# Kernel optimization log

Measured on AMD Instinct MI355X. Metric: run time of the kernel, lower is better.

The kernel has to match this reference:

```python
import jax, jax.numpy as jnp
import numpy as np

B, S = 1024, 64          # batch, num clips (att_size)
R = 1024                 # CG_rnn_size
E = 1024                 # CG_input_encoding_size
CD = 1024                # clip_context_dim
ED = 1024                # event_context_dim
H = 512                  # CG_att_hid_size


def setup_inputs() -> dict:
    key = jax.random.key(0)
    ks = jax.random.split(key, 20)
    s = 0.02
    return {
        "xt": jax.random.normal(ks[0], (B, E), jnp.float32),
        "video": jax.random.normal(ks[1], (B, 1024), jnp.float32),
        "event": jax.random.normal(ks[2], (B, ED), jnp.float32),
        "clip": jax.random.normal(ks[3], (B, S, CD), jnp.float32),
        "clip_mask": jax.random.randint(ks[4], (B, S), 0, 2, jnp.int32),
        "state_h": jax.random.normal(ks[5], (2, B, R), jnp.float32),
        "state_c": jax.random.normal(ks[6], (2, B, R), jnp.float32),
        # LSTMCell 0 (input = event ++ xt -> ED+E)
        "W_ih0": jax.random.normal(ks[7], (4 * R, ED + E), jnp.float32) * s,
        "b_ih0": jnp.zeros((4 * R,), jnp.float32),
        "W_hh0": jax.random.normal(ks[8], (4 * R, R), jnp.float32) * s,
        "b_hh0": jnp.zeros((4 * R,), jnp.float32),
        # LSTMCell 1 (input = att ++ xt -> CD+E)
        "W_ih1": jax.random.normal(ks[9], (4 * R, CD + E), jnp.float32) * s,
        "b_ih1": jnp.zeros((4 * R,), jnp.float32),
        "W_hh1": jax.random.normal(ks[10], (4 * R, R), jnp.float32) * s,
        "b_hh1": jnp.zeros((4 * R,), jnp.float32),
        # Attention params
        "W_ctx": jax.random.normal(ks[11], (H, CD), jnp.float32) * s,
        "b_ctx": jnp.zeros((H,), jnp.float32),
        "W_h2a": jax.random.normal(ks[12], (H, R), jnp.float32) * s,
        "b_h2a": jnp.zeros((H,), jnp.float32),
        "W_alpha": jax.random.normal(ks[13], (1, H), jnp.float32) * s,
        "b_alpha": jnp.zeros((1,), jnp.float32),
    }


def _lstm_cell(x, h, c, W_ih, b_ih, W_hh, b_hh):
    gates = x @ W_ih.T + b_ih + h @ W_hh.T + b_hh  # [B, 4R]
    i, f, g, o = jnp.split(gates, 4, axis=-1)
    i, f, o = jax.nn.sigmoid(i), jax.nn.sigmoid(f), jax.nn.sigmoid(o)
    g = jnp.tanh(g)
    c_new = f * c + i * g
    h_new = o * jnp.tanh(c_new)
    return h_new, c_new


def _attention(h, att_feats, att_mask, W_ctx, b_ctx, W_h2a, b_h2a, W_alpha, b_alpha):
    att = att_feats @ W_ctx.T + b_ctx                 # [B, S, H]
    att_h = h @ W_h2a.T + b_h2a                       # [B, H]
    dot = jnp.tanh(att + att_h[:, None, :])           # [B, S, H]
    scores = (dot @ W_alpha.T + b_alpha)[..., 0]      # [B, S]
    weight = jax.nn.softmax(scores, axis=1)
    m = att_mask.astype(weight.dtype)
    weight = weight * m
    weight = weight / jnp.sum(weight, axis=1, keepdims=True)
    return jnp.einsum('bs,bsd->bd', weight, att_feats)  # [B, CD]


def reference(xt, video, event, clip, clip_mask, state_h, state_c,
              W_ih0, b_ih0, W_hh0, b_hh0, W_ih1, b_ih1, W_hh1, b_hh1,
              W_ctx, b_ctx, W_h2a, b_h2a, W_alpha, b_alpha):
    pre_h1 = state_h[1]
    # stream 0: torch.cat((xt, event), 1)
    h0, c0 = _lstm_cell(jnp.concatenate([xt, event], axis=1),
                        state_h[0], state_c[0], W_ih0, b_ih0, W_hh0, b_hh0)
    att = _attention(pre_h1, clip, clip_mask,
                     W_ctx, b_ctx, W_h2a, b_h2a, W_alpha, b_alpha)
    h1, c1 = _lstm_cell(jnp.concatenate([xt, att], axis=1),
                        state_h[1], state_c[1], W_ih1, b_ih1, W_hh1, b_hh1)
    # dropout layers are identity in eval mode
    output = jnp.concatenate([h0, h1], axis=1)        # [B, 2R]
    new_h = jnp.stack([h0, h1])
    new_c = jnp.stack([c0, c1])
    return output, new_h, new_c
```

## Files before the change

kernel.cpp:

```cpp
#include <hip/hip_runtime.h>

typedef short short8 __attribute__((ext_vector_type(8)));
typedef float floatx4 __attribute__((ext_vector_type(4)));
typedef unsigned short u16;

__device__ __forceinline__ u16 cvt_bf(float x) {
  unsigned u = __float_as_uint(x);
  unsigned r = 0x7FFFu + ((u >> 16) & 1u);
  return (u16)((u + r) >> 16);
}
__device__ __forceinline__ float bf2f(u16 h) {
  return __uint_as_float(((unsigned)h) << 16);
}
__device__ __forceinline__ void gll16(const u16* g, u16* l) {
  __builtin_amdgcn_global_load_lds(
      (__attribute__((address_space(1))) void*)(void*)const_cast<u16*>(g),
      (__attribute__((address_space(3))) void*)(void*)l, 16, 0, 0);
}
__device__ __forceinline__ float fast_tanh(float x) {
  float t = __expf(-2.f * fabsf(x));
  float r = 1.f - 2.f * t / (1.f + t);
  return copysignf(r, x);
}
__device__ __forceinline__ float fast_sigm(float x) {
  return 1.f / (1.f + __expf(-x));
}

#define MAXSEG 13
struct ConvArgs {
  const float* src[MAXSEG];
  u16* dst[MAXSEG];
  unsigned lw[MAXSEG];
  unsigned dstride[MAXSEG];
  unsigned blk0[MAXSEG + 1];
  int nseg;
};
__global__ __launch_bounds__(256)
void convert_seg(ConvArgs a) {
  const unsigned blk = blockIdx.x;
  int s = 0;
  for (int i = 1; i < a.nseg; ++i) if (blk >= a.blk0[i]) s = i;
  const unsigned e0 = (blk - a.blk0[s]) * 2048u + threadIdx.x * 8u;
  short8 p = {};
  u16* d;
  const float* src = a.src[s];
  if (src) {
    const float4 v0 = *(const float4*)(src + e0);
    const float4 v1 = *(const float4*)(src + e0 + 4);
    const unsigned row = e0 >> a.lw[s];
    const unsigned col = e0 & ((1u << a.lw[s]) - 1u);
    d = a.dst[s] + (size_t)row * a.dstride[s] + col;
    p[0] = (short)cvt_bf(v0.x); p[1] = (short)cvt_bf(v0.y);
    p[2] = (short)cvt_bf(v0.z); p[3] = (short)cvt_bf(v0.w);
    p[4] = (short)cvt_bf(v1.x); p[5] = (short)cvt_bf(v1.y);
    p[6] = (short)cvt_bf(v1.z); p[7] = (short)cvt_bf(v1.w);
  } else {
    d = a.dst[s] + e0;
  }
  *(short8*)d = p;
}
__global__ __launch_bounds__(256)
void conv_flat(const float* __restrict__ src, u16* __restrict__ dst) {
  const size_t e = (size_t)blockIdx.x * 2048 + threadIdx.x * 8;
  const float4 v0 = *(const float4*)(src + e);
  const float4 v1 = *(const float4*)(src + e + 4);
  short8 p;
  p[0] = (short)cvt_bf(v0.x); p[1] = (short)cvt_bf(v0.y);
  p[2] = (short)cvt_bf(v0.z); p[3] = (short)cvt_bf(v0.w);
  p[4] = (short)cvt_bf(v1.x); p[5] = (short)cvt_bf(v1.y);
  p[6] = (short)cvt_bf(v1.z); p[7] = (short)cvt_bf(v1.w);
  *(short8*)(dst + e) = p;
}
__global__ __launch_bounds__(256)
void zerof(float* __restrict__ p) { p[blockIdx.x * 256 + threadIdx.x] = 0.f; }

__device__ __forceinline__ void gemm_body(
    const u16* __restrict__ A, int sa, const u16* __restrict__ B, int sb,
    int K, int Mbase, int Nbase, u16* sA, u16* sB, floatx4 (&acc)[4][4])
{
  const int tid = threadIdx.x, lane = tid & 63, w = tid >> 6;
  const int quad = lane >> 4, l15 = lane & 15;
  const int wm = w >> 1, wn = w & 1;
  const int srow = lane >> 3;
  const int sslot = (lane & 7) ^ srow;

  for (int k0 = 0; k0 < K; k0 += 64) {
    __syncthreads();
#pragma unroll
    for (int j = 0; j < 4; ++j) {
      const int c = w + 4 * j;
      const int row = c * 8 + srow;
      gll16(A + (size_t)(Mbase + row) * sa + k0 + sslot * 8, &sA[c * 512]);
      gll16(B + (size_t)(Nbase + row) * sb + k0 + sslot * 8, &sB[c * 512]);
    }
    __syncthreads();
#pragma unroll
    for (int ks = 0; ks < 2; ++ks) {
      short8 af[4], bf[4];
#pragma unroll
      for (int mt = 0; mt < 4; ++mt) {
        const int row = wm * 64 + mt * 16 + l15;
        af[mt] = *(const short8*)&sA[row * 64 + ((ks * 4 + quad) ^ (row & 7)) * 8];
      }
#pragma unroll
      for (int nt = 0; nt < 4; ++nt) {
        const int row = wn * 64 + nt * 16 + l15;
        bf[nt] = *(const short8*)&sB[row * 64 + ((ks * 4 + quad) ^ (row & 7)) * 8];
      }
#pragma unroll
      for (int mt = 0; mt < 4; ++mt)
#pragma unroll
        for (int nt = 0; nt < 4; ++nt)
          acc[mt][nt] = __builtin_amdgcn_mfma_f32_16x16x32_bf16(af[mt], bf[nt], acc[mt][nt], 0, 0, 0);
    }
  }
}

__device__ __forceinline__ void epi_store(
    floatx4 (&acc)[4][4], const float* __restrict__ bias0,
    const float* __restrict__ bias1, float* __restrict__ out,
    int N, int Mbase, int Nbase)
{
  const int tid = threadIdx.x, lane = tid & 63, w = tid >> 6;
  const int quad = lane >> 4, l15 = lane & 15;
  const int wm = w >> 1, wn = w & 1;
#pragma unroll
  for (int nt = 0; nt < 4; ++nt) {
    const int col = Nbase + wn * 64 + nt * 16 + l15;
    const float bc = bias0 ? (bias0[col] + bias1[col]) : 0.f;
#pragma unroll
    for (int mt = 0; mt < 4; ++mt) {
      const int rb = Mbase + wm * 64 + mt * 16 + quad * 4;
#pragma unroll
      for (int r = 0; r < 4; ++r)
        out[(size_t)(rb + r) * N + col] = acc[mt][nt][r] + bc;
    }
  }
}

__device__ __forceinline__ void epi_score(
    floatx4 (&acc)[4][4], const float* __restrict__ atth,
    const float* __restrict__ Walpha, float* __restrict__ scores,
    int Mbase, int Nbase)
{
  const int tid = threadIdx.x, lane = tid & 63, w = tid >> 6;
  const int quad = lane >> 4, l15 = lane & 15;
  const int wm = w >> 1, wn = w & 1;
  const int b = (Mbase + wm * 64) >> 6;
  float rs[4][4] = {};
#pragma unroll
  for (int nt = 0; nt < 4; ++nt) {
    const int col = Nbase + wn * 64 + nt * 16 + l15;
    const float wa = Walpha[col];
    const float ah = atth[(size_t)b * 512 + col];
#pragma unroll
    for (int mt = 0; mt < 4; ++mt)
#pragma unroll
      for (int r = 0; r < 4; ++r)
        rs[mt][r] += wa * fast_tanh(acc[mt][nt][r] + ah);
  }
#pragma unroll
  for (int mt = 0; mt < 4; ++mt)
#pragma unroll
    for (int r = 0; r < 4; ++r) {
      float v = rs[mt][r];
      v += __shfl_xor(v, 1); v += __shfl_xor(v, 2);
      v += __shfl_xor(v, 4); v += __shfl_xor(v, 8);
      if (l15 == 0)
        atomicAdd(&scores[Mbase + wm * 64 + mt * 16 + quad * 4 + r], v);
    }
}

__device__ __forceinline__ void lstm_body(
    const float* __restrict__ gates, const float* __restrict__ g1b,
    const float* __restrict__ cprev, float* __restrict__ out, int st, int blk)
{
  const int idx = blk * 256 + (int)threadIdx.x;
  const int b = idx >> 8;
  const int r4 = (idx & 255) * 4;
  const float* g = gates + (size_t)b * 4096 + r4;
  float4 gi = *(const float4*)g;
  float4 gf = *(const float4*)(g + 1024);
  float4 gg = *(const float4*)(g + 2048);
  float4 go = *(const float4*)(g + 3072);
  if (g1b) {
    const float* h = g1b + (size_t)b * 4096 + r4;
    const float4 hi = *(const float4*)h;
    const float4 hf = *(const float4*)(h + 1024);
    const float4 hg = *(const float4*)(h + 2048);
    const float4 ho = *(const float4*)(h + 3072);
    gi.x += hi.x; gi.y += hi.y; gi.z += hi.z; gi.w += hi.w;
    gf.x += hf.x; gf.y += hf.y; gf.z += hf.z; gf.w += hf.w;
    gg.x += hg.x; gg.y += hg.y; gg.z += hg.z; gg.w += hg.w;
    go.x += ho.x; go.y += ho.y; go.z += ho.z; go.w += ho.w;
  }
  const float4 c = *(const float4*)(cprev + (size_t)b * 1024 + r4);
  float4 cn, hn;
  cn.x = fast_sigm(gf.x) * c.x + fast_sigm(gi.x) * fast_tanh(gg.x);  hn.x = fast_sigm(go.x) * fast_tanh(cn.x);
  cn.y = fast_sigm(gf.y) * c.y + fast_sigm(gi.y) * fast_tanh(gg.y);  hn.y = fast_sigm(go.y) * fast_tanh(cn.y);
  cn.z = fast_sigm(gf.z) * c.z + fast_sigm(gi.z) * fast_tanh(gg.z);  hn.z = fast_sigm(go.z) * fast_tanh(cn.z);
  cn.w = fast_sigm(gf.w) * c.w + fast_sigm(gi.w) * fast_tanh(gg.w);  hn.w = fast_sigm(go.w) * fast_tanh(cn.w);
  *(float4*)(out + (size_t)b * 2048 + st * 1024 + r4) = hn;
  *(float4*)(out + 2097152 + (size_t)st * 1048576 + (size_t)b * 1024 + r4) = hn;
  *(float4*)(out + 4194304 + (size_t)st * 1048576 + (size_t)b * 1024 + r4) = cn;
}

template<int MODE>
__global__ __launch_bounds__(256, 3)
void gemm128(const u16* __restrict__ A, int sa, const u16* __restrict__ B, int sb,
             const float* __restrict__ bias0, const float* __restrict__ bias1,
             float* __restrict__ out, int N, int K,
             const float* __restrict__ atth, const float* __restrict__ Walpha,
             float* __restrict__ scores, int row0,
             const u16* A2, const u16* B2,
             const float* bias0b, const float* bias1b, float* out2)
{
  if (blockIdx.z) { A = A2; B = B2; bias0 = bias0b; bias1 = bias1b; out = out2; }
  __shared__ u16 sA[128 * 64];
  __shared__ u16 sB[128 * 64];
  const int Mbase = blockIdx.y * 128, Nbase = blockIdx.x * 128;
  floatx4 acc[4][4] = {};
  gemm_body(A, sa, B, sb, K, Mbase, Nbase, sA, sB, acc);
  if (MODE == 0) epi_store(acc, bias0, bias1, out, N, Mbase, Nbase);
  else           epi_score(acc, atth, Walpha, scores, row0 + Mbase, Nbase);
}

__global__ __launch_bounds__(256)
void softmax_k(const float* __restrict__ scores, const int* __restrict__ mask,
               float* __restrict__ wbuf)
{
  const int b = blockIdx.x * 4 + (threadIdx.x >> 6);
  const int s = threadIdx.x & 63;
  const float v = scores[b * 64 + s];
  float mx = v;
#pragma unroll
  for (int d = 32; d; d >>= 1) mx = fmaxf(mx, __shfl_xor(mx, d));
  const float e = __expf(v - mx) * (float)mask[b * 64 + s];
  float den = e;
#pragma unroll
  for (int d = 32; d; d >>= 1) den += __shfl_xor(den, d);
  wbuf[b * 64 + s] = e / den;
}

template<int BF>
__global__ __launch_bounds__(128)
void ctx_att(const float* __restrict__ clipf, const u16* __restrict__ clipb,
             const float* __restrict__ wbuf, u16* __restrict__ A1)
{
  __shared__ float w[64];
  const int b = blockIdx.x, tid = threadIdx.x;
  if (tid < 64) w[tid] = wbuf[b * 64 + tid];
  __syncthreads();
  const int c8 = tid * 8;
  float a[8] = {};
  if (BF) {
    const u16* base = clipb + (size_t)b * 65536 + c8;
#pragma unroll 4
    for (int s = 0; s < 64; ++s) {
      const float wt = w[s];
      const short8 c = *(const short8*)(base + (size_t)s * 1024);
#pragma unroll
      for (int j = 0; j < 8; ++j) a[j] += wt * bf2f((u16)c[j]);
    }
  } else {
    const float* base = clipf + (size_t)b * 65536 + c8;
#pragma unroll 4
    for (int s = 0; s < 64; ++s) {
      const float wt = w[s];
      const float4 v0 = *(const float4*)(base + (size_t)s * 1024);
      const float4 v1 = *(const float4*)(base + (size_t)s * 1024 + 4);
      a[0] += wt * v0.x; a[1] += wt * v0.y; a[2] += wt * v0.z; a[3] += wt * v0.w;
      a[4] += wt * v1.x; a[5] += wt * v1.y; a[6] += wt * v1.z; a[7] += wt * v1.w;
    }
  }
  short8 p;
#pragma unroll
  for (int j = 0; j < 8; ++j) p[j] = (short)cvt_bf(a[j]);
  *(short8*)&A1[(size_t)b * 3072 + 1024 + c8] = p;
}

__global__ __launch_bounds__(256)
void lstm_ew(const float* __restrict__ gates, const float* __restrict__ cprev,
             float* __restrict__ out, int st)
{
  lstm_body(gates, nullptr, cprev, out, st, blockIdx.x);
}

__global__ __launch_bounds__(256, 3)
void conv_atth(const float* __restrict__ clip, u16* __restrict__ clipb,
               const u16* __restrict__ A1, const u16* __restrict__ Wh,
               const float* __restrict__ b_h2a, const float* __restrict__ b_ctx,
               float* __restrict__ atth)
{
  __shared__ u16 sA[128 * 64];
  __shared__ u16 sB[128 * 64];
  const int bid = blockIdx.x;
  if (bid < 32) {
    const int Nbase = (bid & 3) * 128, Mbase = (bid >> 2) * 128;
    floatx4 acc[4][4] = {};
    gemm_body(A1 + 2048, 3072, Wh, 1024, 1024, Mbase, Nbase, sA, sB, acc);
    epi_store(acc, b_h2a, b_ctx, atth, 512, Mbase, Nbase);
    return;
  }
  const size_t e = (size_t)(bid - 32) * 2048 + threadIdx.x * 8;
  const float4 v0 = *(const float4*)(clip + e);
  const float4 v1 = *(const float4*)(clip + e + 4);
  short8 p;
  p[0] = (short)cvt_bf(v0.x); p[1] = (short)cvt_bf(v0.y);
  p[2] = (short)cvt_bf(v0.z); p[3] = (short)cvt_bf(v0.w);
  p[4] = (short)cvt_bf(v1.x); p[5] = (short)cvt_bf(v1.y);
  p[6] = (short)cvt_bf(v1.z); p[7] = (short)cvt_bf(v1.w);
  *(short8*)(clipb + e) = p;
}

__global__ __launch_bounds__(256, 3)
void g0score(const u16* __restrict__ A0, const u16* __restrict__ W0,
             const float* __restrict__ bi0, const float* __restrict__ bh0,
             float* __restrict__ gates0,
             const u16* __restrict__ clipb, const u16* __restrict__ Wc,
             const float* __restrict__ atth, const float* __restrict__ Walpha,
             float* __restrict__ scores)
{
  __shared__ u16 sA[128 * 64];
  __shared__ u16 sB[128 * 64];
  floatx4 acc[4][4] = {};
  const int bid = blockIdx.x;
  if (bid < 256) {
    const int Nbase = (bid & 31) * 128, Mbase = (bid >> 5) * 128;
    gemm_body(A0, 3072, W0, 3072, 3072, Mbase, Nbase, sA, sB, acc);
    epi_store(acc, bi0, bh0, gates0, 4096, Mbase, Nbase);
  } else {
    const int t = bid - 256;
    const int Nbase = (t & 3) * 128, Mbase = (t >> 2) * 128;
    gemm_body(clipb, 1024, Wc, 1024, 1024, Mbase, Nbase, sA, sB, acc);
    epi_score(acc, atth, Walpha, scores, Mbase, Nbase);
  }
}

__global__ __launch_bounds__(128)
void sm_ctx(const float* __restrict__ scores, const int* __restrict__ cmask,
            const u16* __restrict__ clipb, u16* __restrict__ A1)
{
  __shared__ float w[64];
  const int b = blockIdx.x, tid = threadIdx.x;
  if (tid < 64) {
    const float v = scores[b * 64 + tid];
    float mx = v;
#pragma unroll
    for (int d = 32; d; d >>= 1) mx = fmaxf(mx, __shfl_xor(mx, d));
    const float e = __expf(v - mx) * (float)cmask[b * 64 + tid];
    float den = e;
#pragma unroll
    for (int d = 32; d; d >>= 1) den += __shfl_xor(den, d);
    w[tid] = e / den;
  }
  __syncthreads();
  const int c8 = tid * 8;
  float a[8] = {};
  const u16* base = clipb + (size_t)b * 65536 + c8;
#pragma unroll 4
  for (int s = 0; s < 64; ++s) {
    const float wt = w[s];
    const short8 c = *(const short8*)(base + (size_t)s * 1024);
#pragma unroll
    for (int j = 0; j < 8; ++j) a[j] += wt * bf2f((u16)c[j]);
  }
  short8 p;
#pragma unroll
  for (int j = 0; j < 8; ++j) p[j] = (short)cvt_bf(a[j]);
  *(short8*)&A1[(size_t)b * 3072 + 1024 + c8] = p;
}

__global__ __launch_bounds__(256, 3)
void g1ew(const u16* __restrict__ A1, const u16* __restrict__ W1,
          const float* __restrict__ bi1, const float* __restrict__ bh1,
          float* __restrict__ g1a, float* __restrict__ g1b,
          const float* __restrict__ gates0, const float* __restrict__ c0p,
          float* __restrict__ out)
{
  __shared__ u16 sA[128 * 64];
  __shared__ u16 sB[128 * 64];
  const int bid = blockIdx.x;
  if (bid < 512) {
    floatx4 acc[4][4] = {};
    const int half = bid >> 8;
    const int t = bid & 255;
    const int Nbase = (t & 31) * 128, Mbase = (t >> 5) * 128;
    const int k0 = half * 1536;
    gemm_body(A1 + k0, 3072, W1 + k0, 3072, 1536, Mbase, Nbase, sA, sB, acc);
    if (half == 0) epi_store(acc, bi1, bh1, g1a, 4096, Mbase, Nbase);
    else           epi_store(acc, nullptr, nullptr, g1b, 4096, Mbase, Nbase);
  } else {
    lstm_body(gates0, nullptr, c0p, out, 0, bid - 512);
  }
}

__global__ __launch_bounds__(256)
void ew1sum(const float* __restrict__ g1a, const float* __restrict__ g1b,
            const float* __restrict__ c1p, float* __restrict__ out)
{
  lstm_body(g1a, g1b, c1p, out, 1, blockIdx.x);
}

extern "C" void kernel_launch(void* const* d_in, const int* in_sizes, int n_in,
                              void* d_out, int out_size, void* d_ws, size_t ws_size,
                              hipStream_t stream) {
  (void)in_sizes; (void)n_in; (void)out_size;
  const float* xt      = (const float*)d_in[0];
  const float* event   = (const float*)d_in[2];
  const float* clip    = (const float*)d_in[3];
  const int*   cmask   = (const int*)d_in[4];
  const float* state_h = (const float*)d_in[5];
  const float* state_c = (const float*)d_in[6];
  const float* W_ih0   = (const float*)d_in[7];
  const float* b_ih0   = (const float*)d_in[8];
  const float* W_hh0   = (const float*)d_in[9];
  const float* b_hh0   = (const float*)d_in[10];
  const float* W_ih1   = (const float*)d_in[11];
  const float* b_ih1   = (const float*)d_in[12];
  const float* W_hh1   = (const float*)d_in[13];
  const float* b_hh1   = (const float*)d_in[14];
  const float* W_ctx   = (const float*)d_in[15];
  const float* b_ctx   = (const float*)d_in[16];
  const float* W_h2a   = (const float*)d_in[17];
  const float* b_h2a   = (const float*)d_in[18];
  const float* W_alpha = (const float*)d_in[19];

  const float* h0p = state_h;
  const float* h1p = state_h + 1048576;
  const float* c0p = state_c;
  const float* c1p = state_c + 1048576;
  float* out = (float*)d_out;

  if (ws_size >= 251920384) {
    char* p = (char*)d_ws;
    float* gates0 = (float*)p; p += 16777216;
    float* g1a    = (float*)p; p += 16777216;
    float* g1b    = (float*)p; p += 16777216;
    u16* A0 = (u16*)p; p += 6291456;
    u16* A1 = (u16*)p; p += 6291456;
    u16* W0 = (u16*)p; p += 25165824;
    u16* W1 = (u16*)p; p += 25165824;
    u16* Wc = (u16*)p; p += 1048576;
    u16* Wh = (u16*)p; p += 1048576;
    u16* clipb = (u16*)p; p += 134217728;
    float* atth   = (float*)p; p += 2097152;
    float* scores = (float*)p;

    ConvArgs ca{};
    {
      const float* srcs[12] = {W_ctx, W_h2a, W_ih0, W_hh0, W_ih1, W_hh1,
                               xt, event, h0p, xt, h1p, nullptr};
      u16* dsts[12] = {Wc, Wh, W0, W0 + 2048, W1, W1 + 2048,
                       A0, A0 + 1024, A0 + 2048, A1, A1 + 2048, (u16*)scores};
      const unsigned lws[12]  = {10, 10, 11, 10, 11, 10, 10, 10, 10, 10, 10, 17};
      const unsigned dstr[12] = {1024, 1024, 3072, 3072, 3072, 3072,
                                 3072, 3072, 3072, 3072, 3072, 0};
      const unsigned nblk[12] = {256, 256, 4096, 2048, 4096, 2048,
                                 512, 512, 512, 512, 512, 64};
      unsigned acc = 0;
      for (int i = 0; i < 12; ++i) {
        ca.src[i] = srcs[i]; ca.dst[i] = dsts[i];
        ca.lw[i] = lws[i]; ca.dstride[i] = dstr[i];
        ca.blk0[i] = acc; acc += nblk[i];
      }
      ca.blk0[12] = acc; ca.nseg = 12;
      convert_seg<<<acc, 256, 0, stream>>>(ca);
    }

    conv_atth<<<32800, 256, 0, stream>>>(clip, clipb, A1, Wh, b_h2a, b_ctx, atth);

    g0score<<<2304, 256, 0, stream>>>(A0, W0, b_ih0, b_hh0, gates0,
                                      clipb, Wc, atth, W_alpha, scores);

    sm_ctx<<<1024, 128, 0, stream>>>(scores, cmask, clipb, A1);

    g1ew<<<1536, 256, 0, stream>>>(A1, W1, b_ih1, b_hh1, g1a, g1b,
                                   gates0, c0p, out);

    ew1sum<<<1024, 256, 0, stream>>>(g1a, g1b, c1p, out);
    return;
  }

  int NC; bool grouped;
  if      (ws_size >= 207618048) { NC = 1; grouped = true;  }
  else if (ws_size >= 106954752) { NC = 4; grouped = true;  }
  else                           { NC = 8; grouped = false; }

  char* p = (char*)d_ws;
  float* gates0 = (float*)p; p += 16777216;
  float* gates1 = gates0;
  if (grouped) { gates1 = (float*)p; p += 16777216; }
  u16* A0 = (u16*)p; p += 6291456;
  u16* A1 = (u16*)p; p += 6291456;
  u16* W0 = (u16*)p; p += 25165824;
  u16* Wc = (u16*)p; p += 1048576;
  u16* Wh = (u16*)p; p += 1048576;
  u16* clipb = (u16*)p;
  u16* W1 = (u16*)p;
  float* atth   = gates0;
  float* wbuf   = gates0 + 524288;
  float* scores = gates0 + 589824;

  ConvArgs ca{};
  {
    const float* srcs[9] = {W_ctx, W_h2a, W_ih0, W_hh0, xt, event, h0p, xt, h1p};
    u16* dsts[9] = {Wc, Wh, W0, W0 + 2048, A0, A0 + 1024, A0 + 2048, A1, A1 + 2048};
    const unsigned lws[9]  = {10, 10, 11, 10, 10, 10, 10, 10, 10};
    const unsigned dstr[9] = {1024, 1024, 3072, 3072, 3072, 3072, 3072, 3072, 3072};
    const unsigned nblk[9] = {256, 256, 4096, 2048, 512, 512, 512, 512, 512};
    unsigned acc = 0;
    for (int i = 0; i < 9; ++i) {
      ca.src[i] = srcs[i]; ca.dst[i] = dsts[i];
      ca.lw[i] = lws[i]; ca.dstride[i] = dstr[i];
      ca.blk0[i] = acc; acc += nblk[i];
    }
    ca.blk0[9] = acc; ca.nseg = 9;
    convert_seg<<<acc, 256, 0, stream>>>(ca);
  }

  zerof<<<256, 256, 0, stream>>>(scores);

  gemm128<0><<<dim3(4, 8, 1), 256, 0, stream>>>(
      A1 + 2048, 3072, Wh, 1024, b_h2a, b_ctx, atth, 512, 1024,
      nullptr, nullptr, nullptr, 0, nullptr, nullptr, nullptr, nullptr, nullptr);

  const int rows = 65536 / NC;
  for (int c = 0; c < NC; ++c) {
    conv_flat<<<rows * 1024 / 2048, 256, 0, stream>>>(clip + (size_t)c * rows * 1024, clipb);
    gemm128<1><<<dim3(4, rows / 128, 1), 256, 0, stream>>>(
        clipb, 1024, Wc, 1024, nullptr, nullptr, nullptr, 512, 1024,
        atth, W_alpha, scores, c * rows,
        nullptr, nullptr, nullptr, nullptr, nullptr);
  }

  softmax_k<<<256, 256, 0, stream>>>(scores, cmask, wbuf);

  if (NC == 1) ctx_att<1><<<1024, 128, 0, stream>>>(clip, clipb, wbuf, A1);
  else         ctx_att<0><<<1024, 128, 0, stream>>>(clip, clipb, wbuf, A1);

  ConvArgs cb{};
  {
    const float* srcs[2] = {W_ih1, W_hh1};
    u16* dsts[2] = {W1, W1 + 2048};
    const unsigned lws[2] = {11, 10};
    const unsigned nblk[2] = {4096, 2048};
    unsigned acc = 0;
    for (int i = 0; i < 2; ++i) {
      cb.src[i] = srcs[i]; cb.dst[i] = dsts[i];
      cb.lw[i] = lws[i]; cb.dstride[i] = 3072;
      cb.blk0[i] = acc; acc += nblk[i];
    }
    cb.blk0[2] = acc; cb.nseg = 2;
    convert_seg<<<acc, 256, 0, stream>>>(cb);
  }

  if (grouped) {
    gemm128<0><<<dim3(32, 8, 2), 256, 0, stream>>>(
        A0, 3072, W0, 3072, b_ih0, b_hh0, gates0, 4096, 3072,
        nullptr, nullptr, nullptr, 0,
        A1, W1, b_ih1, b_hh1, gates1);
    lstm_ew<<<1024, 256, 0, stream>>>(gates0, c0p, out, 0);
    lstm_ew<<<1024, 256, 0, stream>>>(gates1, c1p, out, 1);
  } else {
    gemm128<0><<<dim3(32, 8, 1), 256, 0, stream>>>(
        A0, 3072, W0, 3072, b_ih0, b_hh0, gates0, 4096, 3072,
        nullptr, nullptr, nullptr, 0, nullptr, nullptr, nullptr, nullptr, nullptr);
    lstm_ew<<<1024, 256, 0, stream>>>(gates0, c0p, out, 0);
    gemm128<0><<<dim3(32, 8, 1), 256, 0, stream>>>(
        A1, 3072, W1, 3072, b_ih1, b_hh1, gates0, 4096, 3072,
        nullptr, nullptr, nullptr, 0, nullptr, nullptr, nullptr, nullptr, nullptr);
    lstm_ew<<<1024, 256, 0, stream>>>(gates0, c1p, out, 1);
  }
}
```

Measured before the change: 680.3 us.

## Drop bf16 clip staging; convert fp32 operands inside GEMM tile loads

The separate pass that converted the large clip tensor to bf16 in workspace is removed. The clip-context GEMM now loads fp32 clip and converts it to bf16 while filling shared memory, and the softmax-context kernel reads fp32 clip directly. The h2a GEMM also reads fp32 h1 and W_h2a directly and is merged into the weight-conversion launch, which removes one kernel launch and the W_h2a staging buffer. This cuts a large workspace write plus re-read. In exchange, the fp32 tile loads use register round-trips instead of async global-to-LDS copies, and the context kernel reads twice the bytes per clip element.

Result: slower. 707.5 us (+4.0%).

```diff
diff --git a/kernel.cpp b/kernel.cpp
--- a/kernel.cpp
+++ b/kernel.cpp
@@ -1,6 +1,7 @@
 #include <hip/hip_runtime.h>
 
 typedef short short8 __attribute__((ext_vector_type(8)));
+typedef short sshort4 __attribute__((ext_vector_type(4)));
 typedef float floatx4 __attribute__((ext_vector_type(4)));
 typedef unsigned short u16;
 
@@ -16,6 +17,16 @@
   __builtin_amdgcn_global_load_lds(
       (__attribute__((address_space(1))) void*)(void*)const_cast<u16*>(g),
       (__attribute__((address_space(3))) void*)(void*)l, 16, 0, 0);
+}
+__device__ __forceinline__ short8 load_cvt8(const float* g) {
+  const float4 v0 = *(const float4*)g;
+  const float4 v1 = *(const float4*)(g + 4);
+  short8 p;
+  p[0] = (short)cvt_bf(v0.x); p[1] = (short)cvt_bf(v0.y);
+  p[2] = (short)cvt_bf(v0.z); p[3] = (short)cvt_bf(v0.w);
+  p[4] = (short)cvt_bf(v1.x); p[5] = (short)cvt_bf(v1.y);
+  p[6] = (short)cvt_bf(v1.z); p[7] = (short)cvt_bf(v1.w);
+  return p;
 }
 __device__ __forceinline__ float fast_tanh(float x) {
   float t = __expf(-2.f * fabsf(x));
@@ -35,9 +46,7 @@
   unsigned blk0[MAXSEG + 1];
   int nseg;
 };
-__global__ __launch_bounds__(256)
-void convert_seg(ConvArgs a) {
-  const unsigned blk = blockIdx.x;
+__device__ __forceinline__ void conv_seg_body(const ConvArgs& a, unsigned blk) {
   int s = 0;
   for (int i = 1; i < a.nseg; ++i) if (blk >= a.blk0[i]) s = i;
   const unsigned e0 = (blk - a.blk0[s]) * 2048u + threadIdx.x * 8u;
@@ -45,37 +54,29 @@
   u16* d;
   const float* src = a.src[s];
   if (src) {
-    const float4 v0 = *(const float4*)(src + e0);
-    const float4 v1 = *(const float4*)(src + e0 + 4);
+    p = load_cvt8(src + e0);
     const unsigned row = e0 >> a.lw[s];
     const unsigned col = e0 & ((1u << a.lw[s]) - 1u);
     d = a.dst[s] + (size_t)row * a.dstride[s] + col;
-    p[0] = (short)cvt_bf(v0.x); p[1] = (short)cvt_bf(v0.y);
-    p[2] = (short)cvt_bf(v0.z); p[3] = (short)cvt_bf(v0.w);
-    p[4] = (short)cvt_bf(v1.x); p[5] = (short)cvt_bf(v1.y);
-    p[6] = (short)cvt_bf(v1.z); p[7] = (short)cvt_bf(v1.w);
   } else {
     d = a.dst[s] + e0;
   }
   *(short8*)d = p;
 }
 __global__ __launch_bounds__(256)
+void convert_seg(ConvArgs a) { conv_seg_body(a, blockIdx.x); }
+
+__global__ __launch_bounds__(256)
 void conv_flat(const float* __restrict__ src, u16* __restrict__ dst) {
   const size_t e = (size_t)blockIdx.x * 2048 + threadIdx.x * 8;
-  const float4 v0 = *(const float4*)(src + e);
-  const float4 v1 = *(const float4*)(src + e + 4);
-  short8 p;
-  p[0] = (short)cvt_bf(v0.x); p[1] = (short)cvt_bf(v0.y);
-  p[2] = (short)cvt_bf(v0.z); p[3] = (short)cvt_bf(v0.w);
-  p[4] = (short)cvt_bf(v1.x); p[5] = (short)cvt_bf(v1.y);
-  p[6] = (short)cvt_bf(v1.z); p[7] = (short)cvt_bf(v1.w);
-  *(short8*)(dst + e) = p;
+  *(short8*)(dst + e) = load_cvt8(src + e);
 }
 __global__ __launch_bounds__(256)
 void zerof(float* __restrict__ p) { p[blockIdx.x * 256 + threadIdx.x] = 0.f; }
 
-__device__ __forceinline__ void gemm_body(
-    const u16* __restrict__ A, int sa, const u16* __restrict__ B, int sb,
+template<int AF32, int BF32>
+__device__ __forceinline__ void gemm_body_t(
+    const void* __restrict__ Av, int sa, const void* __restrict__ Bv, int sb,
     int K, int Mbase, int Nbase, u16* sA, u16* sB, floatx4 (&acc)[4][4])
 {
   const int tid = threadIdx.x, lane = tid & 63, w = tid >> 6;
@@ -90,8 +91,18 @@
     for (int j = 0; j < 4; ++j) {
       const int c = w + 4 * j;
       const int row = c * 8 + srow;
-      gll16(A + (size_t)(Mbase + row) * sa + k0 + sslot * 8, &sA[c * 512]);
-      gll16(B + (size_t)(Nbase + row) * sb + k0 + sslot * 8, &sB[c * 512]);
+      if (AF32) {
+        const float* g = (const float*)Av + (size_t)(Mbase + row) * sa + k0 + sslot * 8;
+        *(short8*)&sA[c * 512 + lane * 8] = load_cvt8(g);
+      } else {
+        gll16((const u16*)Av + (size_t)(Mbase + row) * sa + k0 + sslot * 8, &sA[c * 512]);
+      }
+      if (BF32) {
+        const float* g = (const float*)Bv + (size_t)(Nbase + row) * sb + k0 + sslot * 8;
+        *(short8*)&sB[c * 512 + lane * 8] = load_cvt8(g);
+      } else {
+        gll16((const u16*)Bv + (size_t)(Nbase + row) * sb + k0 + sslot * 8, &sB[c * 512]);
+      }
     }
     __syncthreads();
 #pragma unroll
@@ -220,7 +231,7 @@
   __shared__ u16 sB[128 * 64];
   const int Mbase = blockIdx.y * 128, Nbase = blockIdx.x * 128;
   floatx4 acc[4][4] = {};
-  gemm_body(A, sa, B, sb, K, Mbase, Nbase, sA, sB, acc);
+  gemm_body_t<0, 0>(A, sa, B, sb, K, Mbase, Nbase, sA, sB, acc);
   if (MODE == 0) epi_store(acc, bias0, bias1, out, N, Mbase, Nbase);
   else           epi_score(acc, atth, Walpha, scores, row0 + Mbase, Nbase);
 }
@@ -286,11 +297,10 @@
   lstm_body(gates, nullptr, cprev, out, st, blockIdx.x);
 }
 
-__global__ __launch_bounds__(256, 3)
-void conv_atth(const float* __restrict__ clip, u16* __restrict__ clipb,
-               const u16* __restrict__ A1, const u16* __restrict__ Wh,
-               const float* __restrict__ b_h2a, const float* __restrict__ b_ctx,
-               float* __restrict__ atth)
+__global__ __launch_bounds__(256)
+void atth_conv(ConvArgs a, const float* __restrict__ h1p,
+               const float* __restrict__ Wh2a, const float* __restrict__ b_h2a,
+               const float* __restrict__ b_ctx, float* __restrict__ atth)
 {
   __shared__ u16 sA[128 * 64];
   __shared__ u16 sB[128 * 64];
@@ -298,26 +308,18 @@
   if (bid < 32) {
     const int Nbase = (bid & 3) * 128, Mbase = (bid >> 2) * 128;
     floatx4 acc[4][4] = {};
-    gemm_body(A1 + 2048, 3072, Wh, 1024, 1024, Mbase, Nbase, sA, sB, acc);
+    gemm_body_t<1, 1>(h1p, 1024, Wh2a, 1024, 1024, Mbase, Nbase, sA, sB, acc);
     epi_store(acc, b_h2a, b_ctx, atth, 512, Mbase, Nbase);
     return;
   }
-  const size_t e = (size_t)(bid - 32) * 2048 + threadIdx.x * 8;
-  const float4 v0 = *(const float4*)(clip + e);
-  const float4 v1 = *(const float4*)(clip + e + 4);
-  short8 p;
-  p[0] = (short)cvt_bf(v0.x); p[1] = (short)cvt_bf(v0.y);
-  p[2] = (short)cvt_bf(v0.z); p[3] = (short)cvt_bf(v0.w);
-  p[4] = (short)cvt_bf(v1.x); p[5] = (short)cvt_bf(v1.y);
-  p[6] = (short)cvt_bf(v1.z); p[7] = (short)cvt_bf(v1.w);
-  *(short8*)(clipb + e) = p;
+  conv_seg_body(a, bid - 32);
 }
 
 __global__ __launch_bounds__(256, 3)
 void g0score(const u16* __restrict__ A0, const u16* __restrict__ W0,
              const float* __restrict__ bi0, const float* __restrict__ bh0,
              float* __restrict__ gates0,
-             const u16* __restrict__ clipb, const u16* __restrict__ Wc,
+             const float* __restrict__ clip, const u16* __restrict__ Wc,
              const float* __restrict__ atth, const float* __restrict__ Walpha,
              float* __restrict__ scores)
 {
@@ -327,19 +329,19 @@
   const int bid = blockIdx.x;
   if (bid < 256) {
     const int Nbase = (bid & 31) * 128, Mbase = (bid >> 5) * 128;
-    gemm_body(A0, 3072, W0, 3072, 3072, Mbase, Nbase, sA, sB, acc);
+    gemm_body_t<0, 0>(A0, 3072, W0, 3072, 3072, Mbase, Nbase, sA, sB, acc);
     epi_store(acc, bi0, bh0, gates0, 4096, Mbase, Nbase);
   } else {
     const int t = bid - 256;
     const int Nbase = (t & 3) * 128, Mbase = (t >> 2) * 128;
-    gemm_body(clipb, 1024, Wc, 1024, 1024, Mbase, Nbase, sA, sB, acc);
+    gemm_body_t<1, 0>(clip, 1024, Wc, 1024, 1024, Mbase, Nbase, sA, sB, acc);
     epi_score(acc, atth, Walpha, scores, Mbase, Nbase);
   }
 }
 
-__global__ __launch_bounds__(128)
+__global__ __launch_bounds__(256)
 void sm_ctx(const float* __restrict__ scores, const int* __restrict__ cmask,
-            const u16* __restrict__ clipb, u16* __restrict__ A1)
+            const float* __restrict__ clip, u16* __restrict__ A1)
 {
   __shared__ float w[64];
   const int b = blockIdx.x, tid = threadIdx.x;
@@ -355,20 +357,19 @@
     w[tid] = e / den;
   }
   __syncthreads();
-  const int c8 = tid * 8;
-  float a[8] = {};
-  const u16* base = clipb + (size_t)b * 65536 + c8;
+  const int c4 = tid * 4;
+  float a0 = 0.f, a1 = 0.f, a2 = 0.f, a3 = 0.f;
+  const float* base = clip + (size_t)b * 65536 + c4;
 #pragma unroll 4
   for (int s = 0; s < 64; ++s) {
     const float wt = w[s];
-    const short8 c = *(const short8*)(base + (size_t)s * 1024);
-#pragma unroll
-    for (int j = 0; j < 8; ++j) a[j] += wt * bf2f((u16)c[j]);
-  }
-  short8 p;
-#pragma unroll
-  for (int j = 0; j < 8; ++j) p[j] = (short)cvt_bf(a[j]);
-  *(short8*)&A1[(size_t)b * 3072 + 1024 + c8] = p;
+    const float4 v = *(const float4*)(base + (size_t)s * 1024);
+    a0 += wt * v.x; a1 += wt * v.y; a2 += wt * v.z; a3 += wt * v.w;
+  }
+  sshort4 p;
+  p[0] = (short)cvt_bf(a0); p[1] = (short)cvt_bf(a1);
+  p[2] = (short)cvt_bf(a2); p[3] = (short)cvt_bf(a3);
+  *(sshort4*)&A1[(size_t)b * 3072 + 1024 + c4] = p;
 }
 
 __global__ __launch_bounds__(256, 3)
@@ -387,7 +388,7 @@
     const int t = bid & 255;
     const int Nbase = (t & 31) * 128, Mbase = (t >> 5) * 128;
     const int k0 = half * 1536;
-    gemm_body(A1 + k0, 3072, W1 + k0, 3072, 1536, Mbase, Nbase, sA, sB, acc);
+    gemm_body_t<0, 0>(A1 + k0, 3072, W1 + k0, 3072, 1536, Mbase, Nbase, sA, sB, acc);
     if (half == 0) epi_store(acc, bi1, bh1, g1a, 4096, Mbase, Nbase);
     else           epi_store(acc, nullptr, nullptr, g1b, 4096, Mbase, Nbase);
   } else {
@@ -432,7 +433,7 @@
   const float* c1p = state_c + 1048576;
   float* out = (float*)d_out;
 
-  if (ws_size >= 251920384) {
+  if (ws_size >= 116654080) {
     char* p = (char*)d_ws;
     float* gates0 = (float*)p; p += 16777216;
     float* g1a    = (float*)p; p += 16777216;
@@ -442,38 +443,34 @@
     u16* W0 = (u16*)p; p += 25165824;
     u16* W1 = (u16*)p; p += 25165824;
     u16* Wc = (u16*)p; p += 1048576;
-    u16* Wh = (u16*)p; p += 1048576;
-    u16* clipb = (u16*)p; p += 134217728;
     float* atth   = (float*)p; p += 2097152;
     float* scores = (float*)p;
 
     ConvArgs ca{};
     {
-      const float* srcs[12] = {W_ctx, W_h2a, W_ih0, W_hh0, W_ih1, W_hh1,
+      const float* srcs[11] = {W_ctx, W_ih0, W_hh0, W_ih1, W_hh1,
                                xt, event, h0p, xt, h1p, nullptr};
-      u16* dsts[12] = {Wc, Wh, W0, W0 + 2048, W1, W1 + 2048,
+      u16* dsts[11] = {Wc, W0, W0 + 2048, W1, W1 + 2048,
                        A0, A0 + 1024, A0 + 2048, A1, A1 + 2048, (u16*)scores};
-      const unsigned lws[12]  = {10, 10, 11, 10, 11, 10, 10, 10, 10, 10, 10, 17};
-      const unsigned dstr[12] = {1024, 1024, 3072, 3072, 3072, 3072,
+      const unsigned lws[11]  = {10, 11, 10, 11, 10, 10, 10, 10, 10, 10, 17};
+      const unsigned dstr[11] = {1024, 3072, 3072, 3072, 3072,
                                  3072, 3072, 3072, 3072, 3072, 0};
-      const unsigned nblk[12] = {256, 256, 4096, 2048, 4096, 2048,
+      const unsigned nblk[11] = {256, 4096, 2048, 4096, 2048,
                                  512, 512, 512, 512, 512, 64};
       unsigned acc = 0;
-      for (int i = 0; i < 12; ++i) {
+      for (int i = 0; i < 11; ++i) {
         ca.src[i] = srcs[i]; ca.dst[i] = dsts[i];
         ca.lw[i] = lws[i]; ca.dstride[i] = dstr[i];
         ca.blk0[i] = acc; acc += nblk[i];
       }
-      ca.blk0[12] = acc; ca.nseg = 12;
-      convert_seg<<<acc, 256, 0, stream>>>(ca);
-    }
-
-    conv_atth<<<32800, 256, 0, stream>>>(clip, clipb, A1, Wh, b_h2a, b_ctx, atth);
+      ca.blk0[11] = acc; ca.nseg = 11;
+      atth_conv<<<32 + acc, 256, 0, stream>>>(ca, h1p, W_h2a, b_h2a, b_ctx, atth);
+    }
 
     g0score<<<2304, 256, 0, stream>>>(A0, W0, b_ih0, b_hh0, gates0,
-                                      clipb, Wc, atth, W_alpha, scores);
-
-    sm_ctx<<<1024, 128, 0, stream>>>(scores, cmask, clipb, A1);
+                                      clip, Wc, atth, W_alpha, scores);
+
+    sm_ctx<<<1024, 256, 0, stream>>>(scores, cmask, clip, A1);
 
     g1ew<<<1536, 256, 0, stream>>>(A1, W1, b_ih1, b_hh1, g1a, g1b,
                                    gates0, c0p, out);
```
